# Optimization experiments

Hardware: AMD Instinct MI355X
Metric: run time of the kernel (lower is better)

## Reference

```python
import jax, jax.numpy as jnp
import numpy as np
from jax import lax

B, C, H, W = 16, 512, 32, 32
CQ = C // 16


def _conv(x, w, b):
    # NCHW input, OIHW kernel, 3x3 stride-1 'SAME' == torch padding=1
    o = lax.conv_general_dilated(x, w, (1, 1), 'SAME',
                                 dimension_numbers=('NCHW', 'OIHW', 'NCHW'))
    return o + b[None, :, None, None]


def setup_inputs() -> dict:
    key = jax.random.key(0)
    ks = jax.random.split(key, 8)
    fan_q = C * 9
    fan_v = C * 9
    return {
        'x': jax.random.normal(ks[0], (B, C, H, W), jnp.float32),
        'y': jax.random.normal(ks[1], (B, C, H, W), jnp.float32),
        'wq': jax.random.normal(ks[2], (CQ, C, 3, 3), jnp.float32) / np.sqrt(fan_q),
        'bq': jnp.zeros((CQ,), jnp.float32),
        'wk': jax.random.normal(ks[3], (CQ, C, 3, 3), jnp.float32) / np.sqrt(fan_q),
        'bk': jnp.zeros((CQ,), jnp.float32),
        'wv': jax.random.normal(ks[4], (C, C, 3, 3), jnp.float32) / np.sqrt(fan_v),
        'bv': jnp.zeros((C,), jnp.float32),
    }


def reference(x, y, wq, bq, wk, bk, wv, bv):
    b, c, h, w = x.shape
    n = h * w
    q = _conv(x, wq, bq).reshape(b, -1, n)   # (B, CQ, N)
    k = _conv(y, wk, bk).reshape(b, -1, n)   # (B, CQ, N)
    v = _conv(y, wv, bv).reshape(b, c, n)    # (B, C, N)
    # energy[b, i, j] = <q[:, i], k[:, j]>  (unscaled, non-causal)
    energy = jnp.einsum('bdi,bdj->bij', q, k)           # (B, N, N)
    attn = jax.nn.softmax(energy, axis=-1)              # softmax over keys j
    # out[b, c, i] = sum_j v[b, c, j] * attn[b, i, j]
    out = jnp.einsum('bcj,bij->bci', v, attn)           # (B, C, N)
    return out.reshape(b, c, h, w)
```

## Files before the change

### kernel.cpp

```cpp
#include <hip/hip_runtime.h>

#define BB 16
#define CCH 512
#define CQD 32
#define HH 32
#define WW 32
#define NN 1024
#define PH 34

typedef __attribute__((ext_vector_type(8))) _Float16 half8;
typedef __attribute__((ext_vector_type(4))) _Float16 half4;
typedef __attribute__((ext_vector_type(4))) float f32x4;

static __device__ __forceinline__ void gload_lds16(const void* g, void* l) {
    __builtin_amdgcn_global_load_lds(
        (const __attribute__((address_space(1))) unsigned int*)g,
        (__attribute__((address_space(3))) unsigned int*)l, 16, 0, 0);
}

__global__ __launch_bounds__(256) void prep_img_kernel(
    const float* __restrict__ x, const float* __restrict__ y,
    _Float16* __restrict__ xp, _Float16* __restrict__ yp)
{
    const int h = blockIdx.x;
    const int which = blockIdx.y, b = blockIdx.z;
    const float* img = which ? y : x;
    _Float16* row = (which ? yp : xp) + (size_t)(b * PH + h) * PH * CCH;
    const int t = threadIdx.x;
    const int gh = h - 1;

    half8 z;
    #pragma unroll
    for (int u = 0; u < 8; ++u) z[u] = (_Float16)0.f;

    if (gh < 0 || gh >= HH) {
        for (int idx = t; idx < PH * CCH / 8; idx += 256)
            *(half8*)&row[(size_t)idx * 8] = z;
        return;
    }

    __shared__ float X[64][33];
    for (int ci0 = 0; ci0 < CCH; ci0 += 64) {
        __syncthreads();
        #pragma unroll
        for (int i = 0; i < 8; ++i) {
            int ci = i * 8 + (t >> 5), w = t & 31;
            X[ci][w] = img[((size_t)(b * CCH + ci0 + ci) * HH + gh) * WW + w];
        }
        __syncthreads();
        int w = t >> 3, g = t & 7;
        half8 o;
        #pragma unroll
        for (int u = 0; u < 8; ++u) o[u] = (_Float16)X[g * 8 + u][w];
        *(half8*)&row[(size_t)(w + 1) * CCH + ci0 + g * 8] = o;
        if (t < 16) {
            int col = (t < 8) ? 0 : 33;
            *(half8*)&row[(size_t)col * CCH + ci0 + (t & 7) * 8] = z;
        }
    }
}

__global__ __launch_bounds__(256) void prep_w_all_kernel(
    const float* __restrict__ wv, const float* __restrict__ wq,
    const float* __restrict__ wk, _Float16* __restrict__ wvh,
    _Float16* __restrict__ wqkh)
{
    const int bid = blockIdx.x;
    const float* src;
    _Float16* dst;
    int co_src, co_dst;
    if (bid < 512)      { src = wv; co_src = bid;       dst = wvh;  co_dst = bid; }
    else if (bid < 544) { src = wq; co_src = bid - 512; dst = wqkh; co_dst = bid - 512; }
    else                { src = wk; co_src = bid - 544; dst = wqkh; co_dst = 32 + (bid - 544); }
    for (int idx = threadIdx.x; idx < 4608; idx += 256) {
        int tap = idx / 512, ci = idx - tap * 512;
        dst[(size_t)co_dst * 4608 + idx] = (_Float16)src[(size_t)co_src * 4608 + ci * 9 + tap];
    }
}

__global__ __launch_bounds__(256, 2) void conv_v_mfma_kernel(
    const _Float16* __restrict__ yp,
    const _Float16* __restrict__ wvh,
    const float* __restrict__ bvb,
    _Float16* __restrict__ vout)
{
    const int pt  = blockIdx.x;
    const int co0 = blockIdx.y * 64;
    const int b   = blockIdx.z;

    __shared__ __align__(16) _Float16 Wl[64 * 296];
    __shared__ __align__(16) _Float16 Yl[13824];

    const int t    = threadIdx.x;
    const int lane = t & 63;
    const int wv4  = t >> 6;
    const int l15  = lane & 15;
    const int kg   = lane >> 4;

    f32x4 acc[4][4];
    #pragma unroll
    for (int m = 0; m < 4; ++m)
        #pragma unroll
        for (int n = 0; n < 4; ++n) {
            f32x4 z = {0.f, 0.f, 0.f, 0.f};
            acc[m][n] = z;
        }

    const int r0p = pt * 8;
    int bbase[4];
    #pragma unroll
    for (int n = 0; n < 4; ++n) {
        int pxl = wv4 * 64 + n * 16 + l15;
        int rl = pxl >> 5, cl = pxl & 31;
        bbase[n] = (rl * 34 + cl) * 40 + kg * 8;
    }
    int abase[4];
    #pragma unroll
    for (int m = 0; m < 4; ++m)
        abase[m] = (m * 16 + l15) * 296 + kg * 8;

    #pragma unroll 1
    for (int ci0 = 0; ci0 < CCH; ci0 += 32) {
        __syncthreads();
        #pragma unroll
        for (int i = 0; i < 10; ++i) {
            int d = t + i * 256;
            if (d < 2368) {
                int c = d / 37, rem = d - c * 37;
                const _Float16* g = (rem < 36)
                    ? &wvh[(size_t)(co0 + c) * 4608 + (rem >> 2) * 512 + ci0 + (rem & 3) * 8]
                    : wvh;
                gload_lds16(g, (char*)Wl + (size_t)(i * 256 + wv4 * 64) * 16);
            }
        }
        #pragma unroll
        for (int i = 0; i < 7; ++i) {
            int d = t + i * 256;
            if (d < 1728) {
                int rc = d / 5, part = d - rc * 5;
                const _Float16* g = yp;
                if (rc < 340 && part < 4) {
                    int r = rc / 34, c = rc - r * 34;
                    g = &yp[((size_t)(b * PH + r0p + r) * PH + c) * CCH + ci0 + part * 8];
                }
                gload_lds16(g, (char*)Yl + (size_t)(i * 256 + wv4 * 64) * 16);
            }
        }
        __syncthreads();

        #pragma unroll
        for (int tap = 0; tap < 9; ++tap) {
            const int dh = tap / 3, dw = tap % 3;
            half8 a[4], bf[4];
            #pragma unroll
            for (int m = 0; m < 4; ++m)
                a[m] = *(const half8*)&Wl[abase[m] + tap * 32];
            #pragma unroll
            for (int n = 0; n < 4; ++n)
                bf[n] = *(const half8*)&Yl[bbase[n] + (dh * 34 + dw) * 40];
            #pragma unroll
            for (int m = 0; m < 4; ++m)
                #pragma unroll
                for (int n = 0; n < 4; ++n)
                    acc[m][n] = __builtin_amdgcn_mfma_f32_16x16x32_f16(a[m], bf[n], acc[m][n], 0, 0, 0);
        }
    }

    #pragma unroll
    for (int m = 0; m < 4; ++m) {
        #pragma unroll
        for (int reg = 0; reg < 4; ++reg) {
            int co = co0 + m * 16 + kg * 4 + reg;
            float bias = bvb[co];
            #pragma unroll
            for (int n = 0; n < 4; ++n) {
                int px = pt * 256 + wv4 * 64 + n * 16 + l15;
                vout[((size_t)b * CCH + co) * NN + px] = (_Float16)(acc[m][n][reg] + bias);
            }
        }
    }
}

__global__ __launch_bounds__(256, 4) void conv_qk_split_kernel(
    const _Float16* __restrict__ xp,
    const _Float16* __restrict__ yp,
    const _Float16* __restrict__ wqkh,
    float* __restrict__ pbuf)
{
    const int pt    = blockIdx.x >> 2;
    const int ks    = blockIdx.x & 3;
    const int which = blockIdx.y;
    const int b     = blockIdx.z;
    const _Float16* in = which ? yp : xp;

    __shared__ __align__(16) _Float16 Wl[9728];
    __shared__ __align__(16) _Float16 Xl[8192];

    const int t    = threadIdx.x;
    const int lane = t & 63;
    const int w    = t >> 6;
    const int l15  = lane & 15;
    const int kg   = lane >> 4;

    f32x4 acc[2][2];
    #pragma unroll
    for (int m = 0; m < 2; ++m)
        #pragma unroll
        for (int n = 0; n < 2; ++n) {
            f32x4 z = {0.f, 0.f, 0.f, 0.f};
            acc[m][n] = z;
        }

    const int r0p = pt * 4;
    int bbase[2];
    #pragma unroll
    for (int n = 0; n < 2; ++n) {
        int pxl = w * 32 + n * 16 + l15;
        int rl = pxl >> 5, cl = pxl & 31;
        bbase[n] = (rl * 34 + cl) * 40 + kg * 8;
    }
    int abase[2];
    #pragma unroll
    for (int m = 0; m < 2; ++m)
        abase[m] = (m * 16 + l15) * 296 + kg * 8;

    #pragma unroll 1
    for (int cc = 0; cc < 4; ++cc) {
        const int ci0 = ks * 128 + cc * 32;
        __syncthreads();
        #pragma unroll
        for (int i = 0; i < 5; ++i) {
            int d = t + i * 256;
            if (d < 1216) {
                const _Float16* g = wqkh;
                if (d < 1184) {
                    int c = d / 37, rem = d - c * 37;
                    if (rem < 36)
                        g = &wqkh[(size_t)(which * 32 + c) * 4608 + (rem >> 2) * 512 + ci0 + (rem & 3) * 8];
                }
                gload_lds16(g, (char*)Wl + (size_t)(i * 256 + w * 64) * 16);
            }
        }
        #pragma unroll
        for (int i = 0; i < 4; ++i) {
            int d = t + i * 256;
            int rc = d / 5, part = d - rc * 5;
            const _Float16* g = in;
            if (rc < 204 && part < 4) {
                int r = rc / 34, c = rc - r * 34;
                g = &in[((size_t)(b * PH + r0p + r) * PH + c) * CCH + ci0 + part * 8];
            }
            gload_lds16(g, (char*)Xl + (size_t)(i * 256 + w * 64) * 16);
        }
        __syncthreads();

        #pragma unroll
        for (int tap = 0; tap < 9; ++tap) {
            const int dh = tap / 3, dw = tap % 3;
            half8 a[2], bfr[2];
            #pragma unroll
            for (int m = 0; m < 2; ++m)
                a[m] = *(const half8*)&Wl[abase[m] + tap * 32];
            #pragma unroll
            for (int n = 0; n < 2; ++n)
                bfr[n] = *(const half8*)&Xl[bbase[n] + (dh * 34 + dw) * 40];
            #pragma unroll
            for (int m = 0; m < 2; ++m)
                #pragma unroll
                for (int n = 0; n < 2; ++n)
                    acc[m][n] = __builtin_amdgcn_mfma_f32_16x16x32_f16(a[m], bfr[n], acc[m][n], 0, 0, 0);
        }
    }

    float* pb = &pbuf[(((size_t)(ks * 2 + which) * BB + b) * NN) * CQD];
    #pragma unroll
    for (int n = 0; n < 2; ++n) {
        int px = pt * 128 + w * 32 + n * 16 + l15;
        #pragma unroll
        for (int m = 0; m < 2; ++m) {
            float4 o = make_float4(acc[m][n][0], acc[m][n][1], acc[m][n][2], acc[m][n][3]);
            *(float4*)&pb[(size_t)px * CQD + m * 16 + kg * 4] = o;
        }
    }
}

__global__ __launch_bounds__(256) void qk_reduce_kernel(
    const float* __restrict__ pbuf,
    const float* __restrict__ bq, const float* __restrict__ bk,
    _Float16* __restrict__ qh, _Float16* __restrict__ kh)
{
    const int gid   = blockIdx.x * 256 + threadIdx.x;
    const int cog   = gid & 7;
    const int px    = (gid >> 3) & 1023;
    const int b     = (gid >> 13) & 15;
    const int which = gid >> 17;

    const size_t base = (((size_t)which * BB + b) * NN + px) * CQD + cog * 4;
    const size_t kstep = (size_t)2 * BB * NN * CQD;
    float4 s = *(const float4*)&pbuf[base];
    #pragma unroll
    for (int ks = 1; ks < 4; ++ks) {
        float4 p = *(const float4*)&pbuf[base + ks * kstep];
        s.x += p.x; s.y += p.y; s.z += p.z; s.w += p.w;
    }
    const float* bias = which ? bk : bq;
    float4 bv = *(const float4*)&bias[cog * 4];
    half4 o;
    o[0] = (_Float16)(s.x + bv.x);
    o[1] = (_Float16)(s.y + bv.y);
    o[2] = (_Float16)(s.z + bv.z);
    o[3] = (_Float16)(s.w + bv.w);
    _Float16* out = which ? kh : qh;
    *(half4*)&out[((size_t)b * NN + px) * CQD + cog * 4] = o;
}

__global__ __launch_bounds__(256, 2) void attn_fused_kernel(
    const _Float16* __restrict__ qh,
    const _Float16* __restrict__ kh,
    const _Float16* __restrict__ v,
    float* __restrict__ out)
{
    const int wg   = blockIdx.x;
    const int virt = (wg & 7) * 64 + (wg >> 3);
    const int b    = virt >> 5;
    const int i0   = (virt & 31) * 32;

    __shared__ _Float16 Kl[128 * 40];
    __shared__ _Float16 Vl[128 * 136];
    __shared__ _Float16 Pl[32 * 136];
    __shared__ float redm[32][17];
    __shared__ float redl[32][17];

    const int t    = threadIdx.x;
    const int lane = t & 63;
    const int w    = t >> 6;
    const int l15  = lane & 15;
    const int kg   = lane >> 4;

    half8 qb[2];
    #pragma unroll
    for (int n = 0; n < 2; ++n)
        qb[n] = *(const half8*)&qh[((size_t)b * NN + i0 + n * 16 + l15) * CQD + kg * 8];

    float m[2] = {-3.0e38f, -3.0e38f}, l[2] = {0.f, 0.f};
    #pragma unroll 1
    for (int jp = 0; jp < 8; ++jp) {
        __syncthreads();
        #pragma unroll
        for (int r = 0; r < 2; ++r) {
            int idx = t + r * 256;
            int j = idx >> 2, part = idx & 3;
            *(half8*)&Kl[j * 40 + part * 8] =
                *(const half8*)&kh[((size_t)b * NN + jp * 128 + j) * CQD + part * 8];
        }
        __syncthreads();
        #pragma unroll
        for (int ht = 0; ht < 2; ++ht) {
            half8 ak = *(const half8*)&Kl[(ht * 64 + w * 16 + l15) * 40 + kg * 8];
            #pragma unroll
            for (int n = 0; n < 2; ++n) {
                f32x4 s = {0.f, 0.f, 0.f, 0.f};
                s = __builtin_amdgcn_mfma_f32_16x16x32_f16(ak, qb[n], s, 0, 0, 0);
                float tm = fmaxf(fmaxf(s[0], s[1]), fmaxf(s[2], s[3]));
                float m2 = fmaxf(m[n], tm);
                l[n] = l[n] * __expf(m[n] - m2)
                     + __expf(s[0] - m2) + __expf(s[1] - m2)
                     + __expf(s[2] - m2) + __expf(s[3] - m2);
                m[n] = m2;
            }
        }
    }
    __syncthreads();
    #pragma unroll
    for (int n = 0; n < 2; ++n) {
        redm[n * 16 + l15][w * 4 + kg] = m[n];
        redl[n * 16 + l15][w * 4 + kg] = l[n];
    }
    __syncthreads();
    float mr[2], rl[2];
    #pragma unroll
    for (int n = 0; n < 2; ++n) {
        const int i = n * 16 + l15;
        float M = redm[i][0];
        #pragma unroll
        for (int p = 1; p < 16; ++p) M = fmaxf(M, redm[i][p]);
        float L = 0.f;
        #pragma unroll
        for (int p = 0; p < 16; ++p) L += redl[i][p] * __expf(redm[i][p] - M);
        mr[n] = M;
        rl[n] = 1.f / L;
    }

    f32x4 acc[4][2][2];
    #pragma unroll
    for (int cc = 0; cc < 4; ++cc)
        #pragma unroll
        for (int mm = 0; mm < 2; ++mm)
            #pragma unroll
            for (int n = 0; n < 2; ++n) {
                f32x4 z = {0.f, 0.f, 0.f, 0.f};
                acc[cc][mm][n] = z;
            }

    #pragma unroll 1
    for (int jp = 0; jp < 8; ++jp) {
        __syncthreads();
        #pragma unroll
        for (int r = 0; r < 2; ++r) {
            int idx = t + r * 256;
            int j = idx >> 2, part = idx & 3;
            *(half8*)&Kl[j * 40 + part * 8] =
                *(const half8*)&kh[((size_t)b * NN + jp * 128 + j) * CQD + part * 8];
        }
        __syncthreads();
        #pragma unroll
        for (int ht = 0; ht < 2; ++ht) {
            half8 ak = *(const half8*)&Kl[(ht * 64 + w * 16 + l15) * 40 + kg * 8];
            #pragma unroll
            for (int n = 0; n < 2; ++n) {
                f32x4 s = {0.f, 0.f, 0.f, 0.f};
                s = __builtin_amdgcn_mfma_f32_16x16x32_f16(ak, qb[n], s, 0, 0, 0);
                half4 p4;
                #pragma unroll
                for (int reg = 0; reg < 4; ++reg)
                    p4[reg] = (_Float16)(__expf(s[reg] - mr[n]) * rl[n]);
                *(half4*)&Pl[(n * 16 + l15) * 136 + ht * 64 + w * 16 + kg * 4] = p4;
            }
        }
        #pragma unroll
        for (int cc = 0; cc < 4; ++cc) {
            __syncthreads();
            #pragma unroll
            for (int r = 0; r < 8; ++r) {
                int idx = t + r * 256;
                int c = idx >> 4, part = idx & 15;
                *(half8*)&Vl[c * 136 + part * 8] =
                    *(const half8*)&v[((size_t)b * CCH + cc * 128 + c) * NN + jp * 128 + part * 8];
            }
            __syncthreads();
            #pragma unroll
            for (int ks = 0; ks < 4; ++ks) {
                half8 pb[2], va[2];
                #pragma unroll
                for (int n = 0; n < 2; ++n)
                    pb[n] = *(const half8*)&Pl[(n * 16 + l15) * 136 + ks * 32 + kg * 8];
                #pragma unroll
                for (int mm = 0; mm < 2; ++mm)
                    va[mm] = *(const half8*)&Vl[(w * 32 + mm * 16 + l15) * 136 + ks * 32 + kg * 8];
                #pragma unroll
                for (int mm = 0; mm < 2; ++mm)
                    #pragma unroll
                    for (int n = 0; n < 2; ++n)
                        acc[cc][mm][n] = __builtin_amdgcn_mfma_f32_16x16x32_f16(va[mm], pb[n], acc[cc][mm][n], 0, 0, 0);
            }
        }
    }

    #pragma unroll
    for (int cc = 0; cc < 4; ++cc)
        #pragma unroll
        for (int mm = 0; mm < 2; ++mm)
            #pragma unroll
            for (int n = 0; n < 2; ++n)
                #pragma unroll
                for (int reg = 0; reg < 4; ++reg) {
                    int c = cc * 128 + w * 32 + mm * 16 + kg * 4 + reg;
                    out[((size_t)b * CCH + c) * NN + i0 + n * 16 + l15] = acc[cc][mm][n][reg];
                }
}

extern "C" void kernel_launch(void* const* d_in, const int* in_sizes, int n_in,
                              void* d_out, int out_size, void* d_ws, size_t ws_size,
                              hipStream_t stream) {
    const float* x  = (const float*)d_in[0];
    const float* y  = (const float*)d_in[1];
    const float* wq = (const float*)d_in[2];
    const float* bq = (const float*)d_in[3];
    const float* wk = (const float*)d_in[4];
    const float* bk = (const float*)d_in[5];
    const float* wv = (const float*)d_in[6];
    const float* bv = (const float*)d_in[7];
    float* out = (float*)d_out;

    _Float16* qhb = (_Float16*)d_ws;
    _Float16* khb = qhb + (size_t)BB * NN * CQD;
    _Float16* vb   = khb + (size_t)BB * NN * CQD;
    _Float16* ypb  = vb + (size_t)BB * CCH * NN;
    _Float16* xpb  = ypb + (size_t)BB * PH * PH * CCH;
    _Float16* wvh  = xpb + (size_t)BB * PH * PH * CCH;
    _Float16* wqkh = wvh + (size_t)512 * 4608;
    float* pbuf = (float*)vb;

    prep_img_kernel<<<dim3(PH, 2, BB), 256, 0, stream>>>(x, y, xpb, ypb);
    prep_w_all_kernel<<<dim3(576), 256, 0, stream>>>(wv, wq, wk, wvh, wqkh);
    conv_qk_split_kernel<<<dim3(32, 2, BB), 256, 0, stream>>>(xpb, ypb, wqkh, pbuf);
    qk_reduce_kernel<<<dim3(1024), 256, 0, stream>>>(pbuf, bq, bk, qhb, khb);
    conv_v_mfma_kernel<<<dim3(4, 8, BB), 256, 0, stream>>>(ypb, wvh, bv, vb);
    attn_fused_kernel<<<dim3(512), 256, 0, stream>>>(qhb, khb, vb, out);
}
```

Before: 173.7 us.

## Restructure attention kernel with 512-thread blocks and double-buffered async LDS staging

The fused attention kernel now runs 512 threads per block over 64 query rows instead of 32, which halves the grid and doubles reuse of each staged K/V tile. K and V tiles are loaded into LDS with the global_load_lds direct path and double-buffered, so the next tile's load overlaps current MFMA work; LDS buffers are aliased for the reduction scratch. The costs are higher register pressure from the larger accumulator array, fewer blocks (256) on the machine, and extra barriers per V chunk.

```diff
diff --git a/kernel.cpp b/kernel.cpp
--- a/kernel.cpp
+++ b/kernel.cpp
@@ -314,159 +314,174 @@
     *(half4*)&out[((size_t)b * NN + px) * CQD + cog * 4] = o;
 }
 
-__global__ __launch_bounds__(256, 2) void attn_fused_kernel(
+__global__ __launch_bounds__(512, 2) void attn_fused_kernel(
     const _Float16* __restrict__ qh,
     const _Float16* __restrict__ kh,
     const _Float16* __restrict__ v,
     float* __restrict__ out)
 {
     const int wg   = blockIdx.x;
-    const int virt = (wg & 7) * 64 + (wg >> 3);
-    const int b    = virt >> 5;
-    const int i0   = (virt & 31) * 32;
-
-    __shared__ _Float16 Kl[128 * 40];
-    __shared__ _Float16 Vl[128 * 136];
-    __shared__ _Float16 Pl[32 * 136];
-    __shared__ float redm[32][17];
-    __shared__ float redl[32][17];
+    const int virt = (wg & 7) * 32 + (wg >> 3);
+    const int b    = virt >> 4;
+    const int i0   = (virt & 15) * 64;
+
+    __shared__ __align__(16) _Float16 Kl[128 * 40];
+    __shared__ __align__(16) _Float16 Vl[2][64 * 136];
+    __shared__ __align__(16) _Float16 Pl[64 * 136];
+    _Float16* KlA  = (_Float16*)Vl[1];
+    float*    redm = (float*)Vl[0];
+    float*    redl = (float*)Pl;
 
     const int t    = threadIdx.x;
     const int lane = t & 63;
     const int w    = t >> 6;
     const int l15  = lane & 15;
     const int kg   = lane >> 4;
-
-    half8 qb[2];
-    #pragma unroll
-    for (int n = 0; n < 2; ++n)
+    const int mc   = w & 3;
+    const int ih   = w >> 2;
+
+    #define STAGE_K(dst, jp_)                                                   \
+        {                                                                       \
+            _Pragma("unroll")                                                   \
+            for (int i_ = 0; i_ < 2; ++i_) {                                    \
+                int d_ = t + i_ * 512;                                          \
+                if (d_ < 640) {                                                 \
+                    int j_ = d_ / 5, rem_ = d_ - j_ * 5;                        \
+                    const _Float16* g_ = (rem_ < 4)                             \
+                        ? &kh[((size_t)b * NN + (jp_) * 128 + j_) * CQD + rem_ * 8] \
+                        : kh;                                                   \
+                    gload_lds16(g_, (char*)(dst) + (size_t)(i_ * 512 + w * 64) * 16); \
+                }                                                               \
+            }                                                                   \
+        }
+    #define STAGE_V(dst, jp_, cc_)                                              \
+        {                                                                       \
+            _Pragma("unroll")                                                   \
+            for (int i_ = 0; i_ < 3; ++i_) {                                    \
+                int d_ = t + i_ * 512;                                          \
+                if (d_ < 1088) {                                                \
+                    int r_ = d_ / 17, rem_ = d_ - r_ * 17;                      \
+                    const _Float16* g_ = (rem_ < 16)                            \
+                        ? &v[((size_t)b * CCH + (cc_) * 64 + r_) * NN + (jp_) * 128 + rem_ * 8] \
+                        : v;                                                    \
+                    gload_lds16(g_, (char*)(dst) + (size_t)(i_ * 512 + w * 64) * 16); \
+                }                                                               \
+            }                                                                   \
+        }
+
+    half8 qb[4];
+    #pragma unroll
+    for (int n = 0; n < 4; ++n)
         qb[n] = *(const half8*)&qh[((size_t)b * NN + i0 + n * 16 + l15) * CQD + kg * 8];
 
-    float m[2] = {-3.0e38f, -3.0e38f}, l[2] = {0.f, 0.f};
+    float m[4] = {-3.0e38f, -3.0e38f, -3.0e38f, -3.0e38f};
+    float l[4] = {0.f, 0.f, 0.f, 0.f};
+    STAGE_K(Kl, 0);
+    __syncthreads();
     #pragma unroll 1
     for (int jp = 0; jp < 8; ++jp) {
-        __syncthreads();
-        #pragma unroll
-        for (int r = 0; r < 2; ++r) {
-            int idx = t + r * 256;
-            int j = idx >> 2, part = idx & 3;
-            *(half8*)&Kl[j * 40 + part * 8] =
-                *(const half8*)&kh[((size_t)b * NN + jp * 128 + j) * CQD + part * 8];
-        }
-        __syncthreads();
-        #pragma unroll
-        for (int ht = 0; ht < 2; ++ht) {
-            half8 ak = *(const half8*)&Kl[(ht * 64 + w * 16 + l15) * 40 + kg * 8];
-            #pragma unroll
-            for (int n = 0; n < 2; ++n) {
-                f32x4 s = {0.f, 0.f, 0.f, 0.f};
-                s = __builtin_amdgcn_mfma_f32_16x16x32_f16(ak, qb[n], s, 0, 0, 0);
-                float tm = fmaxf(fmaxf(s[0], s[1]), fmaxf(s[2], s[3]));
-                float m2 = fmaxf(m[n], tm);
-                l[n] = l[n] * __expf(m[n] - m2)
-                     + __expf(s[0] - m2) + __expf(s[1] - m2)
-                     + __expf(s[2] - m2) + __expf(s[3] - m2);
-                m[n] = m2;
-            }
-        }
+        const _Float16* kcur = (jp & 1) ? KlA : Kl;
+        _Float16* knxt = (jp & 1) ? Kl : KlA;
+        if (jp < 7) STAGE_K(knxt, jp + 1);
+        half8 ak = *(const half8*)&kcur[(w * 16 + l15) * 40 + kg * 8];
+        #pragma unroll
+        for (int n = 0; n < 4; ++n) {
+            f32x4 s = {0.f, 0.f, 0.f, 0.f};
+            s = __builtin_amdgcn_mfma_f32_16x16x32_f16(ak, qb[n], s, 0, 0, 0);
+            float tm = fmaxf(fmaxf(s[0], s[1]), fmaxf(s[2], s[3]));
+            float m2 = fmaxf(m[n], tm);
+            l[n] = l[n] * __expf(m[n] - m2)
+                 + __expf(s[0] - m2) + __expf(s[1] - m2)
+                 + __expf(s[2] - m2) + __expf(s[3] - m2);
+            m[n] = m2;
+        }
+        __syncthreads();
+    }
+    #pragma unroll
+    for (int n = 0; n < 4; ++n) {
+        redm[(n * 16 + l15) * 33 + w * 4 + kg] = m[n];
+        redl[(n * 16 + l15) * 33 + w * 4 + kg] = l[n];
     }
     __syncthreads();
-    #pragma unroll
-    for (int n = 0; n < 2; ++n) {
-        redm[n * 16 + l15][w * 4 + kg] = m[n];
-        redl[n * 16 + l15][w * 4 + kg] = l[n];
-    }
-    __syncthreads();
-    float mr[2], rl[2];
-    #pragma unroll
-    for (int n = 0; n < 2; ++n) {
+    float mr[4], rl[4];
+    #pragma unroll
+    for (int n = 0; n < 4; ++n) {
         const int i = n * 16 + l15;
-        float M = redm[i][0];
-        #pragma unroll
-        for (int p = 1; p < 16; ++p) M = fmaxf(M, redm[i][p]);
+        float M = redm[i * 33];
+        #pragma unroll
+        for (int p = 1; p < 32; ++p) M = fmaxf(M, redm[i * 33 + p]);
         float L = 0.f;
         #pragma unroll
-        for (int p = 0; p < 16; ++p) L += redl[i][p] * __expf(redm[i][p] - M);
+        for (int p = 0; p < 32; ++p) L += redl[i * 33 + p] * __expf(redm[i * 33 + p] - M);
         mr[n] = M;
         rl[n] = 1.f / L;
     }
-
-    f32x4 acc[4][2][2];
-    #pragma unroll
-    for (int cc = 0; cc < 4; ++cc)
-        #pragma unroll
-        for (int mm = 0; mm < 2; ++mm)
-            #pragma unroll
-            for (int n = 0; n < 2; ++n) {
-                f32x4 z = {0.f, 0.f, 0.f, 0.f};
-                acc[cc][mm][n] = z;
-            }
+    __syncthreads();
+
+    f32x4 acc[8][2];
+    #pragma unroll
+    for (int cc = 0; cc < 8; ++cc)
+        #pragma unroll
+        for (int nl = 0; nl < 2; ++nl) {
+            f32x4 z = {0.f, 0.f, 0.f, 0.f};
+            acc[cc][nl] = z;
+        }
+
+    STAGE_K(Kl, 0);
+    STAGE_V(Vl[0], 0, 0);
+    __syncthreads();
 
     #pragma unroll 1
     for (int jp = 0; jp < 8; ++jp) {
-        __syncthreads();
-        #pragma unroll
-        for (int r = 0; r < 2; ++r) {
-            int idx = t + r * 256;
-            int j = idx >> 2, part = idx & 3;
-            *(half8*)&Kl[j * 40 + part * 8] =
-                *(const half8*)&kh[((size_t)b * NN + jp * 128 + j) * CQD + part * 8];
-        }
-        __syncthreads();
-        #pragma unroll
-        for (int ht = 0; ht < 2; ++ht) {
-            half8 ak = *(const half8*)&Kl[(ht * 64 + w * 16 + l15) * 40 + kg * 8];
-            #pragma unroll
-            for (int n = 0; n < 2; ++n) {
+        {
+            half8 ak = *(const half8*)&Kl[(w * 16 + l15) * 40 + kg * 8];
+            #pragma unroll
+            for (int n = 0; n < 4; ++n) {
                 f32x4 s = {0.f, 0.f, 0.f, 0.f};
                 s = __builtin_amdgcn_mfma_f32_16x16x32_f16(ak, qb[n], s, 0, 0, 0);
                 half4 p4;
                 #pragma unroll
                 for (int reg = 0; reg < 4; ++reg)
                     p4[reg] = (_Float16)(__expf(s[reg] - mr[n]) * rl[n]);
-                *(half4*)&Pl[(n * 16 + l15) * 136 + ht * 64 + w * 16 + kg * 4] = p4;
-            }
-        }
-        #pragma unroll
-        for (int cc = 0; cc < 4; ++cc) {
+                *(half4*)&Pl[(n * 16 + l15) * 136 + w * 16 + kg * 4] = p4;
+            }
+        }
+        __syncthreads();
+        #pragma unroll
+        for (int cc = 0; cc < 8; ++cc) {
+            if (cc < 7) {
+                _Float16* vnxt = (cc & 1) ? (_Float16*)Vl[0] : (_Float16*)Vl[1];
+                STAGE_V(vnxt, jp, cc + 1);
+            } else if (jp < 7) {
+                STAGE_K(Kl, jp + 1);
+                STAGE_V(Vl[0], jp + 1, 0);
+            }
+            const _Float16* vcur = (cc & 1) ? (const _Float16*)Vl[1]
+                                            : (const _Float16*)Vl[0];
+            #pragma unroll
+            for (int ks = 0; ks < 4; ++ks) {
+                half8 va = *(const half8*)&vcur[(mc * 16 + l15) * 136 + ks * 32 + kg * 8];
+                #pragma unroll
+                for (int nl = 0; nl < 2; ++nl) {
+                    half8 pbf = *(const half8*)&Pl[((ih * 2 + nl) * 16 + l15) * 136 + ks * 32 + kg * 8];
+                    acc[cc][nl] = __builtin_amdgcn_mfma_f32_16x16x32_f16(va, pbf, acc[cc][nl], 0, 0, 0);
+                }
+            }
             __syncthreads();
-            #pragma unroll
-            for (int r = 0; r < 8; ++r) {
-                int idx = t + r * 256;
-                int c = idx >> 4, part = idx & 15;
-                *(half8*)&Vl[c * 136 + part * 8] =
-                    *(const half8*)&v[((size_t)b * CCH + cc * 128 + c) * NN + jp * 128 + part * 8];
-            }
-            __syncthreads();
-            #pragma unroll
-            for (int ks = 0; ks < 4; ++ks) {
-                half8 pb[2], va[2];
-                #pragma unroll
-                for (int n = 0; n < 2; ++n)
-                    pb[n] = *(const half8*)&Pl[(n * 16 + l15) * 136 + ks * 32 + kg * 8];
-                #pragma unroll
-                for (int mm = 0; mm < 2; ++mm)
-                    va[mm] = *(const half8*)&Vl[(w * 32 + mm * 16 + l15) * 136 + ks * 32 + kg * 8];
-                #pragma unroll
-                for (int mm = 0; mm < 2; ++mm)
-                    #pragma unroll
-                    for (int n = 0; n < 2; ++n)
-                        acc[cc][mm][n] = __builtin_amdgcn_mfma_f32_16x16x32_f16(va[mm], pb[n], acc[cc][mm][n], 0, 0, 0);
-            }
-        }
-    }
-
-    #pragma unroll
-    for (int cc = 0; cc < 4; ++cc)
-        #pragma unroll
-        for (int mm = 0; mm < 2; ++mm)
-            #pragma unroll
-            for (int n = 0; n < 2; ++n)
-                #pragma unroll
-                for (int reg = 0; reg < 4; ++reg) {
-                    int c = cc * 128 + w * 32 + mm * 16 + kg * 4 + reg;
-                    out[((size_t)b * CCH + c) * NN + i0 + n * 16 + l15] = acc[cc][mm][n][reg];
-                }
+        }
+    }
+
+    #pragma unroll
+    for (int cc = 0; cc < 8; ++cc)
+        #pragma unroll
+        for (int nl = 0; nl < 2; ++nl)
+            #pragma unroll
+            for (int reg = 0; reg < 4; ++reg) {
+                int c = cc * 64 + mc * 16 + kg * 4 + reg;
+                out[((size_t)b * CCH + c) * NN + i0 + ih * 32 + nl * 16 + l15] = acc[cc][nl][reg];
+            }
+    #undef STAGE_K
+    #undef STAGE_V
 }
 
 extern "C" void kernel_launch(void* const* d_in, const int* in_sizes, int n_in,
@@ -496,5 +511,5 @@
     conv_qk_split_kernel<<<dim3(32, 2, BB), 256, 0, stream>>>(xpb, ypb, wqkh, pbuf);
     qk_reduce_kernel<<<dim3(1024), 256, 0, stream>>>(pbuf, bq, bk, qhb, khb);
     conv_v_mfma_kernel<<<dim3(4, 8, BB), 256, 0, stream>>>(ypb, wvh, bv, vb);
-    attn_fused_kernel<<<dim3(512), 256, 0, stream>>>(qhb, khb, vb, out);
-}
+    attn_fused_kernel<<<dim3(256), 512, 0, stream>>>(qhb, khb, vb, out);
+}
```

Result: slower. 202.7 us (+16.7%).

## Double-buffer V tiles with async global-to-LDS loads and read K directly

Applied to the files above, without the earlier changes.

V tiles are now staged into two LDS buffers with global_load_lds, so the next channel chunk loads while the current one feeds MFMAs. The padded 136-wide row layout is kept by issuing a dummy 17th chunk per row. K is read straight from global memory instead of through an LDS tile, which drops two barriers per key block in both passes. The softmax reduction scratch now aliases the P buffer to save LDS. Correctness relies on the barriers also waiting for the asynchronous LDS loads, and LDS use grows with the second V buffer.

```diff
diff --git a/kernel.cpp b/kernel.cpp
--- a/kernel.cpp
+++ b/kernel.cpp
@@ -325,11 +325,10 @@
     const int b    = virt >> 5;
     const int i0   = (virt & 31) * 32;
 
-    __shared__ _Float16 Kl[128 * 40];
-    __shared__ _Float16 Vl[128 * 136];
-    __shared__ _Float16 Pl[32 * 136];
-    __shared__ float redm[32][17];
-    __shared__ float redl[32][17];
+    __shared__ __align__(16) _Float16 Vl[2][128 * 136];
+    __shared__ __align__(16) _Float16 Pl[32 * 136];
+    float* redm = (float*)Pl;
+    float* redl = redm + 32 * 17;
 
     const int t    = threadIdx.x;
     const int lane = t & 63;
@@ -337,6 +336,21 @@
     const int l15  = lane & 15;
     const int kg   = lane >> 4;
 
+    #define STAGE_V(dst, jp_, cc_)                                              \
+        {                                                                       \
+            _Pragma("unroll")                                                   \
+            for (int i_ = 0; i_ < 9; ++i_) {                                    \
+                int d_ = t + i_ * 256;                                          \
+                if (d_ < 2176) {                  \
+                    int r_ = d_ / 17, rem_ = d_ - r_ * 17;                      \
+                    const _Float16* g_ = (rem_ < 16)                            \
+                        ? &v[((size_t)b * CCH + (cc_) * 128 + r_) * NN + (jp_) * 128 + rem_ * 8] \
+                        : v;                                                    \
+                    gload_lds16(g_, (char*)(dst) + (size_t)(i_ * 256 + w * 64) * 16); \
+                }                                                               \
+            }                                                                   \
+        }
+
     half8 qb[2];
     #pragma unroll
     for (int n = 0; n < 2; ++n)
@@ -345,18 +359,10 @@
     float m[2] = {-3.0e38f, -3.0e38f}, l[2] = {0.f, 0.f};
     #pragma unroll 1
     for (int jp = 0; jp < 8; ++jp) {
-        __syncthreads();
-        #pragma unroll
-        for (int r = 0; r < 2; ++r) {
-            int idx = t + r * 256;
-            int j = idx >> 2, part = idx & 3;
-            *(half8*)&Kl[j * 40 + part * 8] =
-                *(const half8*)&kh[((size_t)b * NN + jp * 128 + j) * CQD + part * 8];
-        }
-        __syncthreads();
         #pragma unroll
         for (int ht = 0; ht < 2; ++ht) {
-            half8 ak = *(const half8*)&Kl[(ht * 64 + w * 16 + l15) * 40 + kg * 8];
+            int j = jp * 128 + ht * 64 + w * 16 + l15;
+            half8 ak = *(const half8*)&kh[((size_t)b * NN + j) * CQD + kg * 8];
             #pragma unroll
             for (int n = 0; n < 2; ++n) {
                 f32x4 s = {0.f, 0.f, 0.f, 0.f};
@@ -370,23 +376,22 @@
             }
         }
     }
-    __syncthreads();
     #pragma unroll
     for (int n = 0; n < 2; ++n) {
-        redm[n * 16 + l15][w * 4 + kg] = m[n];
-        redl[n * 16 + l15][w * 4 + kg] = l[n];
+        redm[(n * 16 + l15) * 17 + w * 4 + kg] = m[n];
+        redl[(n * 16 + l15) * 17 + w * 4 + kg] = l[n];
     }
     __syncthreads();
     float mr[2], rl[2];
     #pragma unroll
     for (int n = 0; n < 2; ++n) {
         const int i = n * 16 + l15;
-        float M = redm[i][0];
-        #pragma unroll
-        for (int p = 1; p < 16; ++p) M = fmaxf(M, redm[i][p]);
+        float M = redm[i * 17];
+        #pragma unroll
+        for (int p = 1; p < 16; ++p) M = fmaxf(M, redm[i * 17 + p]);
         float L = 0.f;
         #pragma unroll
-        for (int p = 0; p < 16; ++p) L += redl[i][p] * __expf(redm[i][p] - M);
+        for (int p = 0; p < 16; ++p) L += redl[i * 17 + p] * __expf(redm[i * 17 + p] - M);
         mr[n] = M;
         rl[n] = 1.f / L;
     }
@@ -405,17 +410,11 @@
     #pragma unroll 1
     for (int jp = 0; jp < 8; ++jp) {
         __syncthreads();
-        #pragma unroll
-        for (int r = 0; r < 2; ++r) {
-            int idx = t + r * 256;
-            int j = idx >> 2, part = idx & 3;
-            *(half8*)&Kl[j * 40 + part * 8] =
-                *(const half8*)&kh[((size_t)b * NN + jp * 128 + j) * CQD + part * 8];
-        }
-        __syncthreads();
+        STAGE_V(Vl[0], jp, 0);
         #pragma unroll
         for (int ht = 0; ht < 2; ++ht) {
-            half8 ak = *(const half8*)&Kl[(ht * 64 + w * 16 + l15) * 40 + kg * 8];
+            int j = jp * 128 + ht * 64 + w * 16 + l15;
+            half8 ak = *(const half8*)&kh[((size_t)b * NN + j) * CQD + kg * 8];
             #pragma unroll
             for (int n = 0; n < 2; ++n) {
                 f32x4 s = {0.f, 0.f, 0.f, 0.f};
@@ -430,14 +429,11 @@
         #pragma unroll
         for (int cc = 0; cc < 4; ++cc) {
             __syncthreads();
-            #pragma unroll
-            for (int r = 0; r < 8; ++r) {
-                int idx = t + r * 256;
-                int c = idx >> 4, part = idx & 15;
-                *(half8*)&Vl[c * 136 + part * 8] =
-                    *(const half8*)&v[((size_t)b * CCH + cc * 128 + c) * NN + jp * 128 + part * 8];
-            }
-            __syncthreads();
+            if (cc < 3) {
+                _Float16* vnxt = (_Float16*)Vl[(cc + 1) & 1];
+                STAGE_V(vnxt, jp, cc + 1);
+            }
+            const _Float16* vcur = (const _Float16*)Vl[cc & 1];
             #pragma unroll
             for (int ks = 0; ks < 4; ++ks) {
                 half8 pb[2], va[2];
@@ -446,7 +442,7 @@
                     pb[n] = *(const half8*)&Pl[(n * 16 + l15) * 136 + ks * 32 + kg * 8];
                 #pragma unroll
                 for (int mm = 0; mm < 2; ++mm)
-                    va[mm] = *(const half8*)&Vl[(w * 32 + mm * 16 + l15) * 136 + ks * 32 + kg * 8];
+                    va[mm] = *(const half8*)&vcur[(w * 32 + mm * 16 + l15) * 136 + ks * 32 + kg * 8];
                 #pragma unroll
                 for (int mm = 0; mm < 2; ++mm)
                     #pragma unroll
@@ -467,6 +463,7 @@
                     int c = cc * 128 + w * 32 + mm * 16 + kg * 4 + reg;
                     out[((size_t)b * CCH + c) * NN + i0 + n * 16 + l15] = acc[cc][mm][n][reg];
                 }
+    #undef STAGE_V
 }
 
 extern "C" void kernel_launch(void* const* d_in, const int* in_sizes, int n_in,
```

Result: faster. 169.4 us (median of 2 runs) (-2.5%).
